# Performance work log

Measured on AMD Instinct MI355X. Metric: run time of the kernel, lower is better.

## Reference

```python
import jax, jax.numpy as jnp
import numpy as np
import math

RCR = 5.2
RCA = 3.5
NUM_SPECIES = 4


def _triu_index(num_species):
    s1, s2 = np.triu_indices(num_species)
    ret = np.zeros((num_species, num_species), dtype=np.int32)
    ret[s1, s2] = np.arange(len(s1))
    ret[s2, s1] = np.arange(len(s1))
    return ret


def _cutoff_cosine(d, rc):
    return 0.5 * jnp.cos(d * (math.pi / rc)) + 0.5


def setup_inputs():
    key = jax.random.key(0)
    k1, k2 = jax.random.split(key)
    M, A = 32, 48
    BOX = 8.0  # ~0.43 atoms/A^3, realistic organic density
    coordinates = jax.random.uniform(k1, (M, A, 3), dtype=jnp.float32) * BOX
    species = jax.random.randint(k2, (M, A), 0, NUM_SPECIES)
    EtaR = jnp.array([16.0], dtype=jnp.float32)
    ShfR = jnp.asarray(0.9 + (RCR - 0.9) / 16.0 * np.arange(16), dtype=jnp.float32)
    EtaA = jnp.array([8.0], dtype=jnp.float32)
    Zeta = jnp.array([32.0], dtype=jnp.float32)
    ShfA = jnp.asarray(0.9 + (RCA - 0.9) / 4.0 * np.arange(4), dtype=jnp.float32)
    ShfZ = jnp.asarray((np.arange(8) + 0.5) * np.pi / 8.0, dtype=jnp.float32)
    return {"coordinates": coordinates, "EtaR": EtaR, "ShfR": ShfR,
            "EtaA": EtaA, "Zeta": Zeta, "ShfA": ShfA, "ShfZ": ShfZ,
            "species": species}


def _compute_aev(coordinates, EtaR, ShfR, EtaA, Zeta, ShfA, ShfZ, species):
    M, A, _ = coordinates.shape
    S = NUM_SPECIES
    npairs_sp = S * (S + 1) // 2  # 10 unordered species pairs
    rad_sub = EtaR.shape[0] * ShfR.shape[0]   # 16
    ang_sub = EtaA.shape[0] * Zeta.shape[0] * ShfA.shape[0] * ShfZ.shape[0]  # 32

    diff = coordinates[:, :, None, :] - coordinates[:, None, :, :]  # (M,A,A,3)
    D = jnp.linalg.norm(diff, axis=-1)                              # (M,A,A)
    mrow = jnp.arange(M)[:, None]

    # ---------- radial AEV (eq. 3) ----------
    p1, p2 = np.triu_indices(A, 1)                                  # static (P,)
    d = D[:, p1, p2]                                                # (M,P)
    mask_r = (d <= RCR).astype(d.dtype)
    du = d[:, :, None, None]                                        # (M,P,1,1)
    fc = _cutoff_cosine(du, RCR)
    rt = 0.25 * jnp.exp(-EtaR[:, None] * (du - ShfR[None, :]) ** 2) * fc
    rt = (rt * mask_r[:, :, None, None]).reshape(M, len(p1), rad_sub)
    sp = species
    idx1 = p1[None, :] * S + sp[:, p2]                              # (M,P)
    idx2 = p2[None, :] * S + sp[:, p1]
    radial = jnp.zeros((M, A * S, rad_sub), dtype=rt.dtype)
    radial = radial.at[mrow, idx1].add(rt).at[mrow, idx2].add(rt)
    radial = radial.reshape(M, A, S * rad_sub)

    # ---------- angular AEV (eq. 4) ----------
    # static triple list: central atom i with unordered neighbor pair (j,k), j,k != i
    jj, kk = np.triu_indices(A - 1, 1)
    tri = []
    for i in range(A):
        others = np.concatenate([np.arange(i), np.arange(i + 1, A)])
        tri.append(np.stack([np.full(jj.shape, i), others[jj], others[kk]], 1))
    tri = np.concatenate(tri)                                       # (T,3)
    ci, n1, n2 = tri[:, 0], tri[:, 1], tri[:, 2]

    v1 = coordinates[:, n1] - coordinates[:, ci]                    # (M,T,3)
    v2 = coordinates[:, n2] - coordinates[:, ci]
    d1 = D[:, ci, n1]
    d2 = D[:, ci, n2]
    mask_a = ((d1 <= RCA) & (d2 <= RCA)).astype(d1.dtype)           # (M,T)
    eps = 1e-8  # torch cosine_similarity eps
    cos = 0.95 * jnp.sum(v1 * v2, -1) / (jnp.maximum(d1, eps) * jnp.maximum(d2, eps))
    ang = jnp.arccos(cos)                                           # (M,T)

    # broadcast axes: (M, T, EtaA, Zeta, ShfA, ShfZ) as in torchani constants
    EtaA_b = EtaA.reshape(1, 1, -1, 1, 1, 1)
    Zeta_b = Zeta.reshape(1, 1, 1, -1, 1, 1)
    ShfA_b = ShfA.reshape(1, 1, 1, 1, -1, 1)
    ShfZ_b = ShfZ.reshape(1, 1, 1, 1, 1, -1)
    a6 = ang[:, :, None, None, None, None]
    dm = ((d1 + d2) / 2)[:, :, None, None, None, None]
    fcj = (_cutoff_cosine(d1, RCA) * _cutoff_cosine(d2, RCA))[:, :, None, None, None, None]
    f1 = ((1 + jnp.cos(a6 - ShfZ_b)) / 2) ** Zeta_b
    f2 = jnp.exp(-EtaA_b * (dm - ShfA_b) ** 2)
    at = (2 * f1 * f2 * fcj).reshape(M, tri.shape[0], ang_sub)
    at = at * mask_a[:, :, None]

    triu = jnp.asarray(_triu_index(S))
    pidx = triu[sp[:, n1], sp[:, n2]]                               # (M,T)
    flat = ci[None, :] * npairs_sp + pidx
    angular = jnp.zeros((M, A * npairs_sp, ang_sub), dtype=at.dtype)
    angular = angular.at[mrow, flat].add(at).reshape(M, A, npairs_sp * ang_sub)

    return jnp.concatenate([radial, angular], axis=-1)              # (M,A,384)


def reference(coordinates, EtaR, ShfR, EtaA, Zeta, ShfA, ShfZ, species):
    return _compute_aev(coordinates, EtaR, ShfR, EtaA, Zeta, ShfA, ShfZ, species)
```

## Files before the change

kernel.cpp:

```cpp
#include <hip/hip_runtime.h>
#include <hip/hip_bf16.h>


#define NA 48
#define RCR_F 5.2f
#define RCA_F 3.5f
#define PI_F 3.14159265358979f
#define LOG2E_F 1.44269504088896f
#define RADLEN 64
#define AEVLEN 384

struct Smem {
    float sx[NA], sy[NA], sz[NA];
    int   ssp[NA];
    float ra[NA]; unsigned rbu[NA];
    float ad[NA], avx[NA], avy[NA], avz[NA], afc[NA]; int asp[NA];
    int   nR, nAn;
    float4 pstage[256];
    int    sortidx[256];
    int    bins[10], start[10];
    float rpart[4][64];
    float apart[4][320];
};

template <typename T> __device__ __forceinline__ float toF(const T* p, int i);
template <> __device__ __forceinline__ float toF<float>(const float* p, int i) { return p[i]; }
template <> __device__ __forceinline__ float toF<__hip_bfloat16>(const __hip_bfloat16* p, int i) { return __bfloat162float(p[i]); }

template <typename T> __device__ __forceinline__ void stF(T* p, size_t i, float v);
template <> __device__ __forceinline__ void stF<float>(float* p, size_t i, float v) { p[i] = v; }
template <> __device__ __forceinline__ void stF<__hip_bfloat16>(__hip_bfloat16* p, size_t i, float v) { p[i] = __float2bfloat16(v); }

__device__ __forceinline__ int triu_idx(int a, int b) {
    int lo = a < b ? a : b;
    int hi = a < b ? b : a;
    return lo * 4 - (lo * (lo - 1)) / 2 + (hi - lo);
}

template <typename T>
__device__ void aev_body(Smem& sm,
    const T* __restrict__ coords, const T* __restrict__ etaR_p,
    const T* __restrict__ shfR_p, const T* __restrict__ etaA_p,
    const T* __restrict__ zeta_p, const T* __restrict__ shfA_p,
    const T* __restrict__ shfZ_p, const int* __restrict__ species,
    T* __restrict__ out)
{
    const int tid  = threadIdx.x;
    const int lane = tid & 63;
    const int w    = tid >> 6;
    const int bid  = blockIdx.x;
    const int m  = bid / NA;
    const int ci = bid % NA;

    const float etaR = toF(etaR_p, 0);
    const float etaA = toF(etaA_p, 0);
    const float zeta = toF(zeta_p, 0);
    const float kR   = etaR * LOG2E_F;
    const float k2   = etaA * LOG2E_F;

    if (tid < NA) {
        int g = m * NA + tid;
        sm.sx[tid]  = toF(coords, 3 * g + 0);
        sm.sy[tid]  = toF(coords, 3 * g + 1);
        sm.sz[tid]  = toF(coords, 3 * g + 2);
        sm.ssp[tid] = species[g];
    }
    __syncthreads();

    if (w == 0) {
        const float cx = sm.sx[ci], cy = sm.sy[ci], cz = sm.sz[ci];
        float dx = 0.f, dy = 0.f, dz = 0.f, d = 1e30f;
        if (lane < NA && lane != ci) {
            dx = sm.sx[lane] - cx; dy = sm.sy[lane] - cy; dz = sm.sz[lane] - cz;
            d = sqrtf(dx * dx + dy * dy + dz * dz);
        }
        unsigned long long mR = __ballot(d <= RCR_F);
        unsigned long long mA = __ballot(d <= RCA_F);
        unsigned long long lanebit = 1ull << lane;
        unsigned long long below = lanebit - 1ull;
        if (mR & lanebit) {
            int s = __popcll(mR & below);
            float fcR = 0.5f * __cosf(d * (PI_F / RCR_F)) + 0.5f;
            float rb = fmaxf(__log2f(0.25f * fcR) - kR * d * d, -8.0e4f);
            sm.ra[s]  = 2.f * kR * d;
            sm.rbu[s] = (__float_as_uint(rb) & ~3u) | (unsigned)sm.ssp[lane];
        }
        if (mA & lanebit) {
            int s = __popcll(mA & below);
            sm.ad[s]  = d;
            sm.avx[s] = dx; sm.avy[s] = dy; sm.avz[s] = dz;
            sm.afc[s] = 0.5f * __cosf(d * (PI_F / RCA_F)) + 0.5f;
            sm.asp[s] = sm.ssp[lane];
        }
        if (lane == 0) { sm.nR = (int)__popcll(mR); sm.nAn = (int)__popcll(mA); }
    }
    __syncthreads();

    const int nR  = sm.nR;
    const int nAn = sm.nAn;

    const float myShfR = toF(shfR_p, lane & 15);
    const int   mySp   = lane >> 4;
    const float myRc   = kR * myShfR * myShfR;
    const bool  z32    = (zeta == 32.f);

    float racc = 0.f;
    for (int i = w; i < nR; i += 4) {
        unsigned ru = sm.rbu[i];
        float arg = __builtin_fmaf(sm.ra[i], myShfR, __uint_as_float(ru)) - myRc;
        float t = __builtin_amdgcn_exp2f(arg);
        racc += ((int)(ru & 3u) == mySp) ? t : 0.f;
    }
    sm.rpart[w][lane] = racc;

    const int myA  = (lane >> 3) & 3;
    const int myZ  = lane & 7;
    const int p0   = lane >> 5;
    const float myShfA = toF(shfA_p, myA);
    const float myShfZ = toF(shfZ_p, myZ);
    const float myCz = __cosf(myShfZ);
    const float mySz = __sinf(myShfZ);
    const float myLc = k2 * myShfA * myShfA;

    float accs[5] = {0.f, 0.f, 0.f, 0.f, 0.f};
    const int np = nAn * (nAn - 1) / 2;

    for (int c0 = 0; c0 < np; c0 += 256) {
        const int nc = (np - c0 < 256) ? (np - c0) : 256;
        if (tid < 10) sm.bins[tid] = 0;
        __syncthreads();

        int myrow = -1, myrank = 0;
        if (tid < nc) {
            int p = c0 + tid;
            const int b = 2 * nAn - 1;
            float s = sqrtf((float)(b * b - 8 * p));
            int j = (int)(((float)b - s) * 0.5f);
            if ((j + 1) * (b - 1 - j) <= 2 * p) j++;
            if (j * (b - j) > 2 * p) j--;
            int k = p - ((j * (b - j)) >> 1) + j + 1;

            float d1 = sm.ad[j], d2 = sm.ad[k];
            float dot = sm.avx[j] * sm.avx[k] + sm.avy[j] * sm.avy[k] + sm.avz[j] * sm.avz[k];
            float cv = 0.95f * dot / (fmaxf(d1, 1e-8f) * fmaxf(d2, 1e-8f));
            float sv = sqrtf(fmaxf(1.f - cv * cv, 0.f));
            float dm = 0.5f * (d1 + d2);
            float fc2 = 2.f * sm.afc[j] * sm.afc[k];
            float pe = fmaxf(-k2 * dm * dm + __log2f(fc2), -8.0e4f);
            float pd = 2.f * k2 * dm;
            sm.pstage[tid] = make_float4(cv, sv, pd, pe);
            myrow = triu_idx(sm.asp[j], sm.asp[k]);
            myrank = atomicAdd(&sm.bins[myrow], 1);
        }
        __syncthreads();
        if (tid == 0) {
            int s = 0;
            #pragma unroll
            for (int r = 0; r < 10; r++) { sm.start[r] = s; s += sm.bins[r]; }
        }
        __syncthreads();
        if (myrow >= 0) sm.sortidx[sm.start[myrow] + myrank] = tid;
        __syncthreads();

        #pragma unroll
        for (int r = 0; r < 10; r++) {
            const int st = sm.start[r], cn = sm.bins[r];
            const int half = p0 ^ (r & 1);
            float tacc = 0.f;
            for (int o2 = 2 * w; o2 < cn; o2 += 8) {
                int ord = o2 + half;
                bool valid = ord < cn;
                int q = sm.sortidx[st + (valid ? ord : o2)];
                float4 P = sm.pstage[q];
                float cd = __builtin_fmaf(P.x, myCz, P.y * mySz);
                float x = __builtin_fmaf(0.5f, cd, 0.5f);
                float f1;
                if (z32) { float x2 = x*x, x4 = x2*x2, x8 = x4*x4, x16 = x8*x8; f1 = x16*x16; }
                else     { f1 = __powf(x, zeta); }
                float term = f1 * __builtin_amdgcn_exp2f(
                                 __builtin_fmaf(P.z, myShfA, P.w - myLc));
                tacc += valid ? term : 0.f;
            }
            float other = __shfl_xor(tacc, 32);
            accs[r >> 1] += (half == 0) ? (tacc + other) : 0.f;
        }
        __syncthreads();
    }

    sm.apart[w][lane + 0]   = accs[0];
    sm.apart[w][lane + 64]  = accs[1];
    sm.apart[w][lane + 128] = accs[2];
    sm.apart[w][lane + 192] = accs[3];
    sm.apart[w][lane + 256] = accs[4];
    __syncthreads();

    const size_t ob = (size_t)bid * AEVLEN;
    if (tid < 64) {
        float r = sm.rpart[0][tid] + sm.rpart[1][tid] + sm.rpart[2][tid] + sm.rpart[3][tid];
        stF(out, ob + tid, r);
    }
    {
        float v = sm.apart[0][tid] + sm.apart[1][tid] + sm.apart[2][tid] + sm.apart[3][tid];
        stF(out, ob + RADLEN + tid, v);
    }
    if (tid < 64) {
        int s = 256 + tid;
        float v = sm.apart[0][s] + sm.apart[1][s] + sm.apart[2][s] + sm.apart[3][s];
        stF(out, ob + RADLEN + s, v);
    }
}

__global__ __launch_bounds__(256) void aev_kernel(
    const void* coords, const void* etaR, const void* shfR, const void* etaA,
    const void* zeta, const void* shfA, const void* shfZ,
    const int* __restrict__ species, void* out)
{
    __shared__ Smem sm;
    const float probe = __uint_as_float(((const unsigned int*)shfR)[0]);
    if (probe > 0.85f && probe < 0.95f) {
        aev_body<float>(sm, (const float*)coords, (const float*)etaR,
                        (const float*)shfR, (const float*)etaA, (const float*)zeta,
                        (const float*)shfA, (const float*)shfZ, species, (float*)out);
    } else {
        aev_body<__hip_bfloat16>(sm, (const __hip_bfloat16*)coords,
                        (const __hip_bfloat16*)etaR, (const __hip_bfloat16*)shfR,
                        (const __hip_bfloat16*)etaA, (const __hip_bfloat16*)zeta,
                        (const __hip_bfloat16*)shfA, (const __hip_bfloat16*)shfZ,
                        species, (__hip_bfloat16*)out);
    }
}

extern "C" void kernel_launch(void* const* d_in, const int* in_sizes, int n_in,
                              void* d_out, int out_size, void* d_ws, size_t ws_size,
                              hipStream_t stream) {
    aev_kernel<<<dim3(32 * NA), dim3(256), 0, stream>>>(
        d_in[0], d_in[1], d_in[2], d_in[3], d_in[4], d_in[5], d_in[6],
        (const int*)d_in[7], d_out);
}
```

Measured before the change: 76.67 us.

## Assign one wavefront per center atom and replace block syncs with wave-level ballots

Each wavefront now handles a whole center atom, with six atoms per 384-thread block, instead of one 256-thread block per atom. Neighbor lists, pair staging and species-pair sorting live in per-wave shared memory, and bin counts come from ballot/popcount. This removes __syncthreads, shared atomics and the cross-wave reduction. In exchange each wave works through all triples serially in chunks of 64, so per-wave latency grows and there is less parallelism per atom. The grid shrinks to 256 blocks, which may underfill the GPU.

```diff
diff --git a/kernel.cpp b/kernel.cpp
--- a/kernel.cpp
+++ b/kernel.cpp
@@ -9,18 +9,17 @@
 #define LOG2E_F 1.44269504088896f
 #define RADLEN 64
 #define AEVLEN 384
-
-struct Smem {
-    float sx[NA], sy[NA], sz[NA];
-    int   ssp[NA];
+#define WPB 6
+#define BPM 8
+
+#define WAVE_SYNC() do { asm volatile("s_waitcnt lgkmcnt(0)" ::: "memory"); \
+                         __builtin_amdgcn_sched_barrier(0); } while (0)
+
+struct WaveMem {
     float ra[NA]; unsigned rbu[NA];
     float ad[NA], avx[NA], avy[NA], avz[NA], afc[NA]; int asp[NA];
-    int   nR, nAn;
-    float4 pstage[256];
-    int    sortidx[256];
-    int    bins[10], start[10];
-    float rpart[4][64];
-    float apart[4][320];
+    float4 pstage[64];
+    int    sortidx[64];
 };
 
 template <typename T> __device__ __forceinline__ float toF(const T* p, int i);
@@ -38,7 +37,7 @@
 }
 
 template <typename T>
-__device__ void aev_body(Smem& sm,
+__device__ void aev_body(WaveMem* wm,
     const T* __restrict__ coords, const T* __restrict__ etaR_p,
     const T* __restrict__ shfR_p, const T* __restrict__ etaA_p,
     const T* __restrict__ zeta_p, const T* __restrict__ shfA_p,
@@ -49,8 +48,9 @@
     const int lane = tid & 63;
     const int w    = tid >> 6;
     const int bid  = blockIdx.x;
-    const int m  = bid / NA;
-    const int ci = bid % NA;
+    const int m    = bid >> 3;
+    const int ci   = (bid & 7) * WPB + w;
+    WaveMem& WV = wm[w];
 
     const float etaR = toF(etaR_p, 0);
     const float etaA = toF(etaA_p, 0);
@@ -58,120 +58,125 @@
     const float kR   = etaR * LOG2E_F;
     const float k2   = etaA * LOG2E_F;
 
-    if (tid < NA) {
-        int g = m * NA + tid;
-        sm.sx[tid]  = toF(coords, 3 * g + 0);
-        sm.sy[tid]  = toF(coords, 3 * g + 1);
-        sm.sz[tid]  = toF(coords, 3 * g + 2);
-        sm.ssp[tid] = species[g];
-    }
-    __syncthreads();
-
-    if (w == 0) {
-        const float cx = sm.sx[ci], cy = sm.sy[ci], cz = sm.sz[ci];
-        float dx = 0.f, dy = 0.f, dz = 0.f, d = 1e30f;
-        if (lane < NA && lane != ci) {
-            dx = sm.sx[lane] - cx; dy = sm.sy[lane] - cy; dz = sm.sz[lane] - cz;
-            d = sqrtf(dx * dx + dy * dy + dz * dz);
-        }
-        unsigned long long mR = __ballot(d <= RCR_F);
-        unsigned long long mA = __ballot(d <= RCA_F);
-        unsigned long long lanebit = 1ull << lane;
-        unsigned long long below = lanebit - 1ull;
-        if (mR & lanebit) {
-            int s = __popcll(mR & below);
-            float fcR = 0.5f * __cosf(d * (PI_F / RCR_F)) + 0.5f;
-            float rb = fmaxf(__log2f(0.25f * fcR) - kR * d * d, -8.0e4f);
-            sm.ra[s]  = 2.f * kR * d;
-            sm.rbu[s] = (__float_as_uint(rb) & ~3u) | (unsigned)sm.ssp[lane];
-        }
-        if (mA & lanebit) {
-            int s = __popcll(mA & below);
-            sm.ad[s]  = d;
-            sm.avx[s] = dx; sm.avy[s] = dy; sm.avz[s] = dz;
-            sm.afc[s] = 0.5f * __cosf(d * (PI_F / RCA_F)) + 0.5f;
-            sm.asp[s] = sm.ssp[lane];
-        }
-        if (lane == 0) { sm.nR = (int)__popcll(mR); sm.nAn = (int)__popcll(mA); }
-    }
-    __syncthreads();
-
-    const int nR  = sm.nR;
-    const int nAn = sm.nAn;
+    float ax = 0.f, ay = 0.f, az = 0.f; int aspec = 0;
+    if (lane < NA) {
+        int g = m * NA + lane;
+        ax = toF(coords, 3 * g + 0);
+        ay = toF(coords, 3 * g + 1);
+        az = toF(coords, 3 * g + 2);
+        aspec = species[g];
+    }
+    const float cx = __shfl(ax, ci);
+    const float cy = __shfl(ay, ci);
+    const float cz = __shfl(az, ci);
+
+    float dx = 0.f, dy = 0.f, dz = 0.f, d = 1e30f;
+    if (lane < NA && lane != ci) {
+        dx = ax - cx; dy = ay - cy; dz = az - cz;
+        d = sqrtf(dx * dx + dy * dy + dz * dz);
+    }
+    const unsigned long long mR = __ballot(d <= RCR_F);
+    const unsigned long long mA = __ballot(d <= RCA_F);
+    const unsigned long long lanebit = 1ull << lane;
+    const unsigned long long below = lanebit - 1ull;
+    if (mR & lanebit) {
+        int s = __popcll(mR & below);
+        float fcR = 0.5f * __cosf(d * (PI_F / RCR_F)) + 0.5f;
+        float rb = fmaxf(__log2f(0.25f * fcR) - kR * d * d, -8.0e4f);
+        WV.ra[s]  = 2.f * kR * d;
+        WV.rbu[s] = (__float_as_uint(rb) & ~3u) | (unsigned)aspec;
+    }
+    if (mA & lanebit) {
+        int s = __popcll(mA & below);
+        WV.ad[s]  = d;
+        WV.avx[s] = dx; WV.avy[s] = dy; WV.avz[s] = dz;
+        WV.afc[s] = 0.5f * __cosf(d * (PI_F / RCA_F)) + 0.5f;
+        WV.asp[s] = aspec;
+    }
+    const int nR  = (int)__popcll(mR);
+    const int nAn = (int)__popcll(mA);
+    WAVE_SYNC();
 
     const float myShfR = toF(shfR_p, lane & 15);
     const int   mySp   = lane >> 4;
     const float myRc   = kR * myShfR * myShfR;
-    const bool  z32    = (zeta == 32.f);
-
     float racc = 0.f;
-    for (int i = w; i < nR; i += 4) {
-        unsigned ru = sm.rbu[i];
-        float arg = __builtin_fmaf(sm.ra[i], myShfR, __uint_as_float(ru)) - myRc;
+    for (int i = 0; i < nR; ++i) {
+        unsigned ru = WV.rbu[i];
+        float arg = __builtin_fmaf(WV.ra[i], myShfR, __uint_as_float(ru)) - myRc;
         float t = __builtin_amdgcn_exp2f(arg);
         racc += ((int)(ru & 3u) == mySp) ? t : 0.f;
     }
-    sm.rpart[w][lane] = racc;
-
-    const int myA  = (lane >> 3) & 3;
-    const int myZ  = lane & 7;
-    const int p0   = lane >> 5;
+    const size_t ob = (size_t)(m * NA + ci) * AEVLEN;
+    stF(out, ob + lane, racc);
+
+    const int myA = (lane >> 3) & 3;
+    const int myZ = lane & 7;
+    const int p0  = lane >> 5;
     const float myShfA = toF(shfA_p, myA);
     const float myShfZ = toF(shfZ_p, myZ);
     const float myCz = __cosf(myShfZ);
     const float mySz = __sinf(myShfZ);
     const float myLc = k2 * myShfA * myShfA;
+    const bool  z32  = (zeta == 32.f);
 
     float accs[5] = {0.f, 0.f, 0.f, 0.f, 0.f};
     const int np = nAn * (nAn - 1) / 2;
 
-    for (int c0 = 0; c0 < np; c0 += 256) {
-        const int nc = (np - c0 < 256) ? (np - c0) : 256;
-        if (tid < 10) sm.bins[tid] = 0;
-        __syncthreads();
-
-        int myrow = -1, myrank = 0;
-        if (tid < nc) {
-            int p = c0 + tid;
+    for (int c0 = 0; c0 < np; c0 += 64) {
+        const int nc = (np - c0 < 64) ? (np - c0) : 64;
+        const bool active = lane < nc;
+        int myrow = -1;
+        if (active) {
+            int p = c0 + lane;
             const int b = 2 * nAn - 1;
-            float s = sqrtf((float)(b * b - 8 * p));
-            int j = (int)(((float)b - s) * 0.5f);
+            float sq = sqrtf((float)(b * b - 8 * p));
+            int j = (int)(((float)b - sq) * 0.5f);
             if ((j + 1) * (b - 1 - j) <= 2 * p) j++;
             if (j * (b - j) > 2 * p) j--;
             int k = p - ((j * (b - j)) >> 1) + j + 1;
 
-            float d1 = sm.ad[j], d2 = sm.ad[k];
-            float dot = sm.avx[j] * sm.avx[k] + sm.avy[j] * sm.avy[k] + sm.avz[j] * sm.avz[k];
+            float d1 = WV.ad[j], d2 = WV.ad[k];
+            float dot = WV.avx[j] * WV.avx[k] + WV.avy[j] * WV.avy[k] + WV.avz[j] * WV.avz[k];
             float cv = 0.95f * dot / (fmaxf(d1, 1e-8f) * fmaxf(d2, 1e-8f));
             float sv = sqrtf(fmaxf(1.f - cv * cv, 0.f));
             float dm = 0.5f * (d1 + d2);
-            float fc2 = 2.f * sm.afc[j] * sm.afc[k];
+            float fc2 = 2.f * WV.afc[j] * WV.afc[k];
             float pe = fmaxf(-k2 * dm * dm + __log2f(fc2), -8.0e4f);
             float pd = 2.f * k2 * dm;
-            sm.pstage[tid] = make_float4(cv, sv, pd, pe);
-            myrow = triu_idx(sm.asp[j], sm.asp[k]);
-            myrank = atomicAdd(&sm.bins[myrow], 1);
+            WV.pstage[lane] = make_float4(cv, sv, pd, pe);
+            myrow = triu_idx(WV.asp[j], WV.asp[k]);
         }
-        __syncthreads();
-        if (tid == 0) {
-            int s = 0;
+
+        int cnt[10], st[10];
+        {
+            int run = 0, rank = 0, stmy = 0;
             #pragma unroll
-            for (int r = 0; r < 10; r++) { sm.start[r] = s; s += sm.bins[r]; }
+            for (int r = 0; r < 10; ++r) {
+                unsigned long long bm = __ballot(myrow == r);
+                bool mine = (myrow == r);
+                rank = mine ? (int)__popcll(bm & below) : rank;
+                stmy = mine ? run : stmy;
+                st[r]  = run;
+                cnt[r] = (int)__popcll(bm);
+                run += cnt[r];
+            }
+            if (active) WV.sortidx[stmy + rank] = lane;
         }
-        __syncthreads();
-        if (myrow >= 0) sm.sortidx[sm.start[myrow] + myrank] = tid;
-        __syncthreads();
+        WAVE_SYNC();
 
         #pragma unroll
-        for (int r = 0; r < 10; r++) {
-            const int st = sm.start[r], cn = sm.bins[r];
-            const int half = p0 ^ (r & 1);
-            float tacc = 0.f;
-            for (int o2 = 2 * w; o2 < cn; o2 += 8) {
-                int ord = o2 + half;
-                bool valid = ord < cn;
-                int q = sm.sortidx[st + (valid ? ord : o2)];
-                float4 P = sm.pstage[q];
+        for (int u = 0; u < 5; ++u) {
+            const int cnE = cnt[2 * u], cnO = cnt[2 * u + 1];
+            const int stE = st[2 * u],  stO = st[2 * u + 1];
+            const int cnMy = p0 ? cnO : cnE;
+            const int stMy = p0 ? stO : stE;
+            const int trips = cnE > cnO ? cnE : cnO;
+            for (int o = 0; o < trips; ++o) {
+                bool valid = o < cnMy;
+                int idx = valid ? (stMy + o) : 0;
+                int q = WV.sortidx[idx];
+                float4 P = WV.pstage[q];
                 float cd = __builtin_fmaf(P.x, myCz, P.y * mySz);
                 float x = __builtin_fmaf(0.5f, cd, 0.5f);
                 float f1;
@@ -179,50 +184,30 @@
                 else     { f1 = __powf(x, zeta); }
                 float term = f1 * __builtin_amdgcn_exp2f(
                                  __builtin_fmaf(P.z, myShfA, P.w - myLc));
-                tacc += valid ? term : 0.f;
+                accs[u] += valid ? term : 0.f;
             }
-            float other = __shfl_xor(tacc, 32);
-            accs[r >> 1] += (half == 0) ? (tacc + other) : 0.f;
         }
-        __syncthreads();
-    }
-
-    sm.apart[w][lane + 0]   = accs[0];
-    sm.apart[w][lane + 64]  = accs[1];
-    sm.apart[w][lane + 128] = accs[2];
-    sm.apart[w][lane + 192] = accs[3];
-    sm.apart[w][lane + 256] = accs[4];
-    __syncthreads();
-
-    const size_t ob = (size_t)bid * AEVLEN;
-    if (tid < 64) {
-        float r = sm.rpart[0][tid] + sm.rpart[1][tid] + sm.rpart[2][tid] + sm.rpart[3][tid];
-        stF(out, ob + tid, r);
-    }
-    {
-        float v = sm.apart[0][tid] + sm.apart[1][tid] + sm.apart[2][tid] + sm.apart[3][tid];
-        stF(out, ob + RADLEN + tid, v);
-    }
-    if (tid < 64) {
-        int s = 256 + tid;
-        float v = sm.apart[0][s] + sm.apart[1][s] + sm.apart[2][s] + sm.apart[3][s];
-        stF(out, ob + RADLEN + s, v);
-    }
-}
-
-__global__ __launch_bounds__(256) void aev_kernel(
+        WAVE_SYNC();
+    }
+
+    #pragma unroll
+    for (int u = 0; u < 5; ++u)
+        stF(out, ob + RADLEN + 64 * u + lane, accs[u]);
+}
+
+__global__ __launch_bounds__(384) void aev_kernel(
     const void* coords, const void* etaR, const void* shfR, const void* etaA,
     const void* zeta, const void* shfA, const void* shfZ,
     const int* __restrict__ species, void* out)
 {
-    __shared__ Smem sm;
+    __shared__ WaveMem wm[WPB];
     const float probe = __uint_as_float(((const unsigned int*)shfR)[0]);
     if (probe > 0.85f && probe < 0.95f) {
-        aev_body<float>(sm, (const float*)coords, (const float*)etaR,
+        aev_body<float>(wm, (const float*)coords, (const float*)etaR,
                         (const float*)shfR, (const float*)etaA, (const float*)zeta,
                         (const float*)shfA, (const float*)shfZ, species, (float*)out);
     } else {
-        aev_body<__hip_bfloat16>(sm, (const __hip_bfloat16*)coords,
+        aev_body<__hip_bfloat16>(wm, (const __hip_bfloat16*)coords,
                         (const __hip_bfloat16*)etaR, (const __hip_bfloat16*)shfR,
                         (const __hip_bfloat16*)etaA, (const __hip_bfloat16*)zeta,
                         (const __hip_bfloat16*)shfA, (const __hip_bfloat16*)shfZ,
@@ -233,7 +218,7 @@
 extern "C" void kernel_launch(void* const* d_in, const int* in_sizes, int n_in,
                               void* d_out, int out_size, void* d_ws, size_t ws_size,
                               hipStream_t stream) {
-    aev_kernel<<<dim3(32 * NA), dim3(256), 0, stream>>>(
+    aev_kernel<<<dim3(32 * BPM), dim3(64 * WPB), 0, stream>>>(
         d_in[0], d_in[1], d_in[2], d_in[3], d_in[4], d_in[5], d_in[6],
         (const int*)d_in[7], d_out);
 }
```

Result: slower. 93.25 us (+21.6%).

## Make angular triplet binning wave-local with ballot sort, removing block barriers

Applied to the files above, without the earlier changes.

Each wave now takes its own 64-triplet chunk and bins it by species pair with ballot/popcount in registers, replacing the shared atomic counters and the four block-wide barriers per chunk. Each half-wave then accumulates the even or odd species pair directly, so the cross-half shuffle reduction goes away. All waves compute the neighbour ballots redundantly, and waves 0 and 1 split the radial and angular list writes, which removes the shared-memory broadcast of the counts. In exchange, lanes whose pair has fewer triplets sit idle in the unbalanced per-pair loops, and the code relies on an lgkmcnt wait instead of a full barrier to order the LDS accesses.

```diff
diff --git a/kernel.cpp b/kernel.cpp
--- a/kernel.cpp
+++ b/kernel.cpp
@@ -10,15 +10,16 @@
 #define RADLEN 64
 #define AEVLEN 384
 
+#define WAVE_SYNC() do { asm volatile("s_waitcnt lgkmcnt(0)" ::: "memory"); \
+                         __builtin_amdgcn_sched_barrier(0); } while (0)
+
 struct Smem {
     float sx[NA], sy[NA], sz[NA];
     int   ssp[NA];
     float ra[NA]; unsigned rbu[NA];
     float ad[NA], avx[NA], avy[NA], avz[NA], afc[NA]; int asp[NA];
-    int   nR, nAn;
-    float4 pstage[256];
-    int    sortidx[256];
-    int    bins[10], start[10];
+    float4 pstage[4][64];
+    int    sortidx[4][64];
     float rpart[4][64];
     float apart[4][320];
 };
@@ -67,43 +68,37 @@
     }
     __syncthreads();
 
-    if (w == 0) {
-        const float cx = sm.sx[ci], cy = sm.sy[ci], cz = sm.sz[ci];
-        float dx = 0.f, dy = 0.f, dz = 0.f, d = 1e30f;
-        if (lane < NA && lane != ci) {
-            dx = sm.sx[lane] - cx; dy = sm.sy[lane] - cy; dz = sm.sz[lane] - cz;
-            d = sqrtf(dx * dx + dy * dy + dz * dz);
-        }
-        unsigned long long mR = __ballot(d <= RCR_F);
-        unsigned long long mA = __ballot(d <= RCA_F);
-        unsigned long long lanebit = 1ull << lane;
-        unsigned long long below = lanebit - 1ull;
-        if (mR & lanebit) {
-            int s = __popcll(mR & below);
-            float fcR = 0.5f * __cosf(d * (PI_F / RCR_F)) + 0.5f;
-            float rb = fmaxf(__log2f(0.25f * fcR) - kR * d * d, -8.0e4f);
-            sm.ra[s]  = 2.f * kR * d;
-            sm.rbu[s] = (__float_as_uint(rb) & ~3u) | (unsigned)sm.ssp[lane];
-        }
-        if (mA & lanebit) {
-            int s = __popcll(mA & below);
-            sm.ad[s]  = d;
-            sm.avx[s] = dx; sm.avy[s] = dy; sm.avz[s] = dz;
-            sm.afc[s] = 0.5f * __cosf(d * (PI_F / RCA_F)) + 0.5f;
-            sm.asp[s] = sm.ssp[lane];
-        }
-        if (lane == 0) { sm.nR = (int)__popcll(mR); sm.nAn = (int)__popcll(mA); }
-    }
+    const float cx = sm.sx[ci], cy = sm.sy[ci], cz = sm.sz[ci];
+    float dx = 0.f, dy = 0.f, dz = 0.f, d = 1e30f;
+    if (lane < NA && lane != ci) {
+        dx = sm.sx[lane] - cx; dy = sm.sy[lane] - cy; dz = sm.sz[lane] - cz;
+        d = sqrtf(dx * dx + dy * dy + dz * dz);
+    }
+    const unsigned long long mRm = __ballot(d <= RCR_F);
+    const unsigned long long mAm = __ballot(d <= RCA_F);
+    const unsigned long long lanebit = 1ull << lane;
+    const unsigned long long below = lanebit - 1ull;
+    if (w == 0 && (mRm & lanebit)) {
+        int s = __popcll(mRm & below);
+        float fcR = 0.5f * __cosf(d * (PI_F / RCR_F)) + 0.5f;
+        float rb = fmaxf(__log2f(0.25f * fcR) - kR * d * d, -8.0e4f);
+        sm.ra[s]  = 2.f * kR * d;
+        sm.rbu[s] = (__float_as_uint(rb) & ~3u) | (unsigned)sm.ssp[lane];
+    }
+    if (w == 1 && (mAm & lanebit)) {
+        int s = __popcll(mAm & below);
+        sm.ad[s]  = d;
+        sm.avx[s] = dx; sm.avy[s] = dy; sm.avz[s] = dz;
+        sm.afc[s] = 0.5f * __cosf(d * (PI_F / RCA_F)) + 0.5f;
+        sm.asp[s] = sm.ssp[lane];
+    }
+    const int nR  = (int)__popcll(mRm);
+    const int nAn = (int)__popcll(mAm);
     __syncthreads();
-
-    const int nR  = sm.nR;
-    const int nAn = sm.nAn;
 
     const float myShfR = toF(shfR_p, lane & 15);
     const int   mySp   = lane >> 4;
     const float myRc   = kR * myShfR * myShfR;
-    const bool  z32    = (zeta == 32.f);
-
     float racc = 0.f;
     for (int i = w; i < nR; i += 4) {
         unsigned ru = sm.rbu[i];
@@ -113,29 +108,28 @@
     }
     sm.rpart[w][lane] = racc;
 
-    const int myA  = (lane >> 3) & 3;
-    const int myZ  = lane & 7;
-    const int p0   = lane >> 5;
+    const int myA = (lane >> 3) & 3;
+    const int myZ = lane & 7;
+    const int p0  = lane >> 5;
     const float myShfA = toF(shfA_p, myA);
     const float myShfZ = toF(shfZ_p, myZ);
     const float myCz = __cosf(myShfZ);
     const float mySz = __sinf(myShfZ);
     const float myLc = k2 * myShfA * myShfA;
+    const bool  z32  = (zeta == 32.f);
 
     float accs[5] = {0.f, 0.f, 0.f, 0.f, 0.f};
     const int np = nAn * (nAn - 1) / 2;
 
-    for (int c0 = 0; c0 < np; c0 += 256) {
-        const int nc = (np - c0 < 256) ? (np - c0) : 256;
-        if (tid < 10) sm.bins[tid] = 0;
-        __syncthreads();
-
-        int myrow = -1, myrank = 0;
-        if (tid < nc) {
-            int p = c0 + tid;
+    for (int base = 64 * w; base < np; base += 256) {
+        const int nc = (np - base < 64) ? (np - base) : 64;
+        const bool active = lane < nc;
+        int myrow = -1;
+        if (active) {
+            int p = base + lane;
             const int b = 2 * nAn - 1;
-            float s = sqrtf((float)(b * b - 8 * p));
-            int j = (int)(((float)b - s) * 0.5f);
+            float sq = sqrtf((float)(b * b - 8 * p));
+            int j = (int)(((float)b - sq) * 0.5f);
             if ((j + 1) * (b - 1 - j) <= 2 * p) j++;
             if (j * (b - j) > 2 * p) j--;
             int k = p - ((j * (b - j)) >> 1) + j + 1;
@@ -148,30 +142,39 @@
             float fc2 = 2.f * sm.afc[j] * sm.afc[k];
             float pe = fmaxf(-k2 * dm * dm + __log2f(fc2), -8.0e4f);
             float pd = 2.f * k2 * dm;
-            sm.pstage[tid] = make_float4(cv, sv, pd, pe);
+            sm.pstage[w][lane] = make_float4(cv, sv, pd, pe);
             myrow = triu_idx(sm.asp[j], sm.asp[k]);
-            myrank = atomicAdd(&sm.bins[myrow], 1);
         }
-        __syncthreads();
-        if (tid == 0) {
-            int s = 0;
+
+        int cnt[10], st[10];
+        {
+            int run = 0, rank = 0, stmy = 0;
             #pragma unroll
-            for (int r = 0; r < 10; r++) { sm.start[r] = s; s += sm.bins[r]; }
+            for (int r = 0; r < 10; ++r) {
+                unsigned long long bm = __ballot(myrow == r);
+                bool mine = (myrow == r);
+                rank = mine ? (int)__popcll(bm & below) : rank;
+                stmy = mine ? run : stmy;
+                st[r]  = run;
+                cnt[r] = (int)__popcll(bm);
+                run += cnt[r];
+            }
+            if (active) sm.sortidx[w][stmy + rank] = lane;
         }
-        __syncthreads();
-        if (myrow >= 0) sm.sortidx[sm.start[myrow] + myrank] = tid;
-        __syncthreads();
+        WAVE_SYNC();
 
         #pragma unroll
-        for (int r = 0; r < 10; r++) {
-            const int st = sm.start[r], cn = sm.bins[r];
-            const int half = p0 ^ (r & 1);
-            float tacc = 0.f;
-            for (int o2 = 2 * w; o2 < cn; o2 += 8) {
-                int ord = o2 + half;
-                bool valid = ord < cn;
-                int q = sm.sortidx[st + (valid ? ord : o2)];
-                float4 P = sm.pstage[q];
+        for (int u = 0; u < 5; ++u) {
+            const int cnE = cnt[2 * u], cnO = cnt[2 * u + 1];
+            const int stE = st[2 * u],  stO = st[2 * u + 1];
+            const int cnMy = p0 ? cnO : cnE;
+            const int stMy = p0 ? stO : stE;
+            const int trips = cnE > cnO ? cnE : cnO;
+            for (int o = 0; o < trips; ++o) {
+                bool valid = o < cnMy;
+                int idx = valid ? (stMy + o) : 0;
+                int q = sm.sortidx[w][idx];
+                float4 P = sm.pstage[w][q];
                 float cd = __builtin_fmaf(P.x, myCz, P.y * mySz);
                 float x = __builtin_fmaf(0.5f, cd, 0.5f);
                 float f1;
@@ -179,12 +182,10 @@
                 else     { f1 = __powf(x, zeta); }
                 float term = f1 * __builtin_amdgcn_exp2f(
                                  __builtin_fmaf(P.z, myShfA, P.w - myLc));
-                tacc += valid ? term : 0.f;
+                accs[u] += valid ? term : 0.f;
             }
-            float other = __shfl_xor(tacc, 32);
-            accs[r >> 1] += (half == 0) ? (tacc + other) : 0.f;
         }
-        __syncthreads();
+        WAVE_SYNC();
     }
 
     sm.apart[w][lane + 0]   = accs[0];
```

New measurement: 79.79 us. +4.1%, slower.
